# Optimization experiments

Hardware: AMD Instinct MI355X
Metric: run time of the kernel (lower is better)

The kernel has to match this reference:

```python
import jax, jax.numpy as jnp
import numpy as np

N_NODES = 100000
N_EDGES = 1600000
IN_DIM, HID, N_CLS = 128, 256, 40


def setup_inputs() -> dict:
    key = jax.random.key(0)
    ks = jax.random.split(key, 8)
    x = jax.random.normal(ks[0], (N_NODES, IN_DIM), dtype=jnp.float32)
    edge_index = jax.random.randint(ks[1], (2, N_EDGES), 0, N_NODES, dtype=jnp.int64)
    def glorot(k, shape):
        scale = (6.0 / (shape[0] + shape[1])) ** 0.5
        return jax.random.uniform(k, shape, jnp.float32, -scale, scale)
    return {
        "x": x,
        "edge_index": edge_index,
        "W1": glorot(ks[2], (IN_DIM, HID)),
        "b1": jnp.zeros((HID,), jnp.float32),
        "W2": glorot(ks[3], (HID, HID)),
        "b2": jnp.zeros((HID,), jnp.float32),
        "W3": glorot(ks[4], (HID, N_CLS)),
        "b3": jnp.zeros((N_CLS,), jnp.float32),
    }


def _gcn_norm(edge_index, num_nodes):
    # Add self-loops, then symmetric normalization deg^-1/2 * deg^-1/2 (PyG GCNConv).
    loops = jnp.arange(num_nodes, dtype=edge_index.dtype)
    src = jnp.concatenate([edge_index[0], loops])
    dst = jnp.concatenate([edge_index[1], loops])
    deg = jax.ops.segment_sum(jnp.ones_like(dst, dtype=jnp.float32), dst,
                              num_segments=num_nodes)
    dinv = jnp.where(deg > 0, jax.lax.rsqrt(deg), 0.0)
    norm = dinv[src] * dinv[dst]  # [E + N]
    return src, dst, norm


def _gcn_conv(x, W, b, src, dst, norm, num_nodes):
    h = x @ W                       # [N, out] dense GEMM first (out <= in here is fine)
    msg = h[src] * norm[:, None]    # irregular gather, [E+N, out]
    out = jax.ops.segment_sum(msg, dst, num_segments=num_nodes)  # scatter-add
    return out + b


def reference(x, edge_index, W1, b1, W2, b2, W3, b3):
    n = x.shape[0]
    src, dst, norm = _gcn_norm(edge_index, n)
    h = jax.nn.relu(_gcn_conv(x, W1, b1, src, dst, norm, n))
    h = jax.nn.relu(_gcn_conv(h, W2, b2, src, dst, norm, n))
    h = _gcn_conv(h, W3, b3, src, dst, norm, n)
    return jax.nn.log_softmax(h, axis=1)
```

## Files before the change

kernel.cpp:

```cpp
#include <hip/hip_runtime.h>
#include <stdint.h>
#include <math.h>

#define N_NODES 100000
#define N_EDGES 1600000
#define IN_DIM 128
#define HID 256
#define N_CLS 40
#define NBKT 391
#define NPB 391

typedef __attribute__((ext_vector_type(8))) short short8;
typedef __attribute__((ext_vector_type(4))) float f32x4;

__device__ __forceinline__ unsigned short f2bf(float f) {
  unsigned b = __float_as_uint(f);
  b += 0x7fffu + ((b >> 16) & 1u);
  return (unsigned short)(b >> 16);
}
__device__ __forceinline__ float bflo(unsigned u) { return __uint_as_float(u << 16); }
__device__ __forceinline__ float bfhi(unsigned u) { return __uint_as_float(u & 0xffff0000u); }

__device__ __forceinline__ int load_idx(const void* eidx, int flag, size_t pos) {
  return flag ? (int)((const long long*)eidx)[pos] : ((const int*)eidx)[pos];
}

__global__ __launch_bounds__(512) void k_pre0(const unsigned int* __restrict__ ew,
                                              int* __restrict__ flag,
                                              int* __restrict__ hist) {
  int t = threadIdx.x;
  for (int k = t; k < NBKT; k += 512) hist[k] = 0;
  __shared__ unsigned int sh[512];
  unsigned int v = 0;
  for (int k = t; k < 4096; k += 512) v |= ew[2 * k + 1];
  sh[t] = v;
  __syncthreads();
  for (int s = 256; s > 0; s >>= 1) {
    if (t < s) sh[t] |= sh[t + s];
    __syncthreads();
  }
  if (t == 0) flag[0] = (sh[0] == 0u) ? 1 : 0;
}

__global__ __launch_bounds__(256) void k_hist(const void* __restrict__ eidx,
                                              const int* __restrict__ flagp,
                                              int* __restrict__ hist) {
  __shared__ int lh[NBKT];
  int t = threadIdx.x;
  for (int k = t; k < NBKT; k += 256) lh[k] = 0;
  __syncthreads();
  int flag = flagp[0];
  int base = blockIdx.x * 4096;
#pragma unroll
  for (int j = 0; j < 16; j++) {
    int e = base + j * 256 + t;
    if (e < N_EDGES) {
      int d = load_idx(eidx, flag, (size_t)N_EDGES + e);
      atomicAdd(&lh[d >> 8], 1);
    }
  }
  __syncthreads();
  for (int k = t; k < NBKT; k += 256) {
    int c = lh[k];
    if (c) atomicAdd(&hist[k], c);
  }
}

__global__ __launch_bounds__(512) void k_bscan(const int* __restrict__ hist,
                                               int* __restrict__ bucket_start,
                                               int* __restrict__ bucket_cursor) {
  __shared__ int sh[512];
  int t = threadIdx.x;
  int v = (t < NBKT) ? hist[t] : 0;
  sh[t] = v;
  __syncthreads();
  for (int off = 1; off < 512; off <<= 1) {
    int u = (t >= off) ? sh[t - off] : 0;
    __syncthreads();
    sh[t] += u;
    __syncthreads();
  }
  if (t < NBKT) {
    bucket_start[t + 1] = sh[t];
    bucket_cursor[t] = sh[t] - v;
  }
  if (t == 0) bucket_start[0] = 0;
}

__global__ __launch_bounds__(256) void k_part(const void* __restrict__ eidx,
                                              const int* __restrict__ flagp,
                                              int* __restrict__ bucket_cursor,
                                              uint2* __restrict__ bpairs) {
  __shared__ int lcur[NBKT];
  int t = threadIdx.x;
  for (int k = t; k < NBKT; k += 256) lcur[k] = 0;
  __syncthreads();
  int flag = flagp[0];
  int base = blockIdx.x * 4096;
#pragma unroll
  for (int j = 0; j < 16; j++) {
    int e = base + j * 256 + t;
    if (e < N_EDGES) {
      int d = load_idx(eidx, flag, (size_t)N_EDGES + e);
      atomicAdd(&lcur[d >> 8], 1);
    }
  }
  __syncthreads();
  for (int k = t; k < NBKT; k += 256) {
    int c = lcur[k];
    int g = c ? atomicAdd(&bucket_cursor[k], c) : 0;
    lcur[k] = g;
  }
  __syncthreads();
#pragma unroll
  for (int j = 0; j < 16; j++) {
    int e = base + j * 256 + t;
    if (e < N_EDGES) {
      int s = load_idx(eidx, flag, e);
      int d = load_idx(eidx, flag, (size_t)N_EDGES + e);
      int p = atomicAdd(&lcur[d >> 8], 1);
      bpairs[p] = make_uint2((unsigned)s, (unsigned)d);
    }
  }
}

__global__ __launch_bounds__(256) void k_bsort(const uint2* __restrict__ bpairs,
                                               const int* __restrict__ bucket_start,
                                               int* __restrict__ row_start,
                                               float* __restrict__ dinv,
                                               int* __restrict__ csr_src) {
  __shared__ int ldeg[256], lsum[256], lcur[256];
  int b = blockIdx.x, t = threadIdx.x;
  int d0 = b << 8;
  int nd = min(256, N_NODES - d0);
  int base = bucket_start[b];
  int n = bucket_start[b + 1] - base;
  ldeg[t] = 0;
  __syncthreads();
  for (int i = t; i < n; i += 256) {
    uint2 p = bpairs[base + i];
    atomicAdd(&ldeg[p.y - d0], 1);
  }
  __syncthreads();
  lsum[t] = ldeg[t];
  __syncthreads();
  for (int off = 1; off < 256; off <<= 1) {
    int v = (t >= off) ? lsum[t - off] : 0;
    __syncthreads();
    lsum[t] += v;
    __syncthreads();
  }
  int excl = lsum[t] - ldeg[t];
  if (t < nd) {
    row_start[d0 + t] = base + excl;
    dinv[d0 + t] = rsqrtf((float)(ldeg[t] + 1));
  }
  lcur[t] = base + excl;
  __syncthreads();
  for (int i = t; i < n; i += 256) {
    uint2 p = bpairs[base + i];
    int pos = atomicAdd(&lcur[p.y - d0], 1);
    csr_src[pos] = (int)p.x;
  }
  if (b == 0 && t == 0) row_start[N_NODES] = N_EDGES;
}

__global__ __launch_bounds__(256) void k_wprep(const float* __restrict__ W1,
                                               const float* __restrict__ W2,
                                               const float* __restrict__ W3,
                                               unsigned short* __restrict__ T1,
                                               unsigned short* __restrict__ T2,
                                               unsigned short* __restrict__ T3) {
  int idx = blockIdx.x * 256 + threadIdx.x;
  if (idx < 32768) {
    int n = idx >> 7, k = idx & 127;
    T1[idx] = f2bf(W1[(size_t)k * HID + n]);
  } else if (idx < 98304) {
    int j = idx - 32768;
    int n = j >> 8, k = j & 255;
    T2[j] = f2bf(W2[(size_t)k * HID + n]);
  } else if (idx < 131072) {
    int j = idx - 98304;
    int n = j >> 8, k = j & 255;
    T3[j] = f2bf((n < N_CLS) ? W3[(size_t)k * N_CLS + n] : 0.f);
  }
}

__global__ __launch_bounds__(256) void k_qx(const float* __restrict__ x,
                                            const float* __restrict__ dinv,
                                            unsigned short* __restrict__ xq,
                                            float* __restrict__ sw_x) {
  int node = (blockIdx.x << 2) + (threadIdx.x >> 6);
  int lane = threadIdx.x & 63;
  if (node >= N_NODES) return;
  float2 v = ((const float2*)x)[(size_t)node * 64 + lane];
  float m = fmaxf(fabsf(v.x), fabsf(v.y));
  for (int off = 32; off; off >>= 1) m = fmaxf(m, __shfl_down(m, off));
  m = __shfl(m, 0);
  float inv = (m > 0.f) ? 127.f / m : 0.f;
  int q0 = __float2int_rn(v.x * inv);
  int q1 = __float2int_rn(v.y * inv);
  xq[(size_t)node * 64 + lane] = (unsigned short)((q0 & 0xff) | ((q1 & 0xff) << 8));
  if (lane == 0) sw_x[node] = dinv[node] * ((m > 0.f) ? m / 127.f : 0.f);
}

__device__ __forceinline__ void up4a(unsigned v, float w,
                                     float& a0, float& a1, float& a2, float& a3) {
  float f0, f1, f2, f3;
  asm("v_cvt_f32_ubyte0 %0, %1" : "=v"(f0) : "v"(v));
  asm("v_cvt_f32_ubyte1 %0, %1" : "=v"(f1) : "v"(v));
  asm("v_cvt_f32_ubyte2 %0, %1" : "=v"(f2) : "v"(v));
  asm("v_cvt_f32_ubyte3 %0, %1" : "=v"(f3) : "v"(v));
  a0 = fmaf(f0, w, a0);
  a1 = fmaf(f1, w, a1);
  a2 = fmaf(f2, w, a2);
  a3 = fmaf(f3, w, a3);
}

__global__ __launch_bounds__(256, 8) void k_agg256i(const unsigned* __restrict__ tbl,
                                                    uint2* __restrict__ out,
                                                    const float* __restrict__ dinv,
                                                    const float* __restrict__ swp,
                                                    const int* __restrict__ row_start,
                                                    const int* __restrict__ csr_src) {
  int node = (blockIdx.x << 2) + (threadIdx.x >> 6);
  int lane = threadIdx.x & 63;
  if (node >= N_NODES) return;
  node = __builtin_amdgcn_readfirstlane(node);
  const char* tb = (const char*)tbl;
  const char* sb = (const char*)swp;
  int l4 = lane << 2;
  int h4 = (lane >= 32) ? 4 : 0;
  float d = dinv[node];
  float ws = *(const float*)(sb + ((size_t)(unsigned)node << 3) + h4);
  unsigned v0 = *(const unsigned*)(tb + ((size_t)(unsigned)node << 8) + l4);
  float a0 = 0.f, a1 = 0.f, a2 = 0.f, a3 = 0.f;

  int e0 = __builtin_amdgcn_readfirstlane(row_start[node]);
  int e1 = __builtin_amdgcn_readfirstlane(row_start[node + 1]);
  const int* ep = csr_src + e0;
  int n = e1 - e0;

  int idx[8];
  if (n > 0) {
#pragma unroll
    for (int j = 0; j < 8; j++) idx[j] = __builtin_amdgcn_readfirstlane(ep[min(j, n - 1)]);
  }
  up4a(v0, ws, a0, a1, a2, a3);

  int k = 0;
  for (; k + 8 <= n; k += 8) {
    int cur[8];
#pragma unroll
    for (int j = 0; j < 8; j++) cur[j] = idx[j];
    if (k + 8 < n) {
#pragma unroll
      for (int j = 0; j < 8; j++)
        idx[j] = __builtin_amdgcn_readfirstlane(ep[min(k + 8 + j, n - 1)]);
    }
    unsigned r[8];
    float w[8];
#pragma unroll
    for (int j = 0; j < 8; j++)
      r[j] = *(const unsigned*)(tb + ((size_t)(unsigned)cur[j] << 8) + l4);
#pragma unroll
    for (int j = 0; j < 8; j++)
      w[j] = *(const float*)(sb + ((size_t)(unsigned)cur[j] << 3) + h4);
#pragma unroll
    for (int j = 0; j < 8; j++) up4a(r[j], w[j], a0, a1, a2, a3);
  }
  if (k < n) {
    unsigned r[8];
    float w[8];
#pragma unroll
    for (int j = 0; j < 8; j++)
      r[j] = *(const unsigned*)(tb + ((size_t)(unsigned)idx[j] << 8) + l4);
#pragma unroll
    for (int j = 0; j < 8; j++) {
      float wv = *(const float*)(sb + ((size_t)(unsigned)idx[j] << 3) + h4);
      w[j] = (k + j < n) ? wv : 0.f;
    }
#pragma unroll
    for (int j = 0; j < 8; j++) up4a(r[j], w[j], a0, a1, a2, a3);
  }

  a0 *= d; a1 *= d; a2 *= d; a3 *= d;
  uint2 o;
  o.x = f2bf(a0) | ((unsigned)f2bf(a1) << 16);
  o.y = f2bf(a2) | ((unsigned)f2bf(a3) << 16);
  out[(size_t)node * 64 + lane] = o;
}

__global__ __launch_bounds__(256, 8) void k_agg128i(const unsigned short* __restrict__ tbl,
                                                    unsigned* __restrict__ out,
                                                    const float* __restrict__ dinv,
                                                    const float* __restrict__ sw,
                                                    const int* __restrict__ row_start,
                                                    const int* __restrict__ csr_src) {
  int node = (blockIdx.x << 2) + (threadIdx.x >> 6);
  int lane = threadIdx.x & 63;
  if (node >= N_NODES) return;
  node = __builtin_amdgcn_readfirstlane(node);
  const char* tb = (const char*)tbl;
  int l2 = lane << 1;
  float d = dinv[node];
  float ws = sw[node];
  unsigned short v0 = *(const unsigned short*)(tb + ((size_t)(unsigned)node << 7) + l2);

  int e0 = __builtin_amdgcn_readfirstlane(row_start[node]);
  int e1 = __builtin_amdgcn_readfirstlane(row_start[node + 1]);
  const int* ep = csr_src + e0;
  int n = e1 - e0;

  int idx[8];
  if (n > 0) {
#pragma unroll
    for (int j = 0; j < 8; j++) idx[j] = __builtin_amdgcn_readfirstlane(ep[min(j, n - 1)]);
  }
  float a0 = (float)(signed char)(v0 & 0xff) * ws;
  float a1 = (float)(signed char)(v0 >> 8) * ws;

  int k = 0;
  for (; k + 8 <= n; k += 8) {
    int cur[8];
#pragma unroll
    for (int j = 0; j < 8; j++) cur[j] = idx[j];
    if (k + 8 < n) {
#pragma unroll
      for (int j = 0; j < 8; j++)
        idx[j] = __builtin_amdgcn_readfirstlane(ep[min(k + 8 + j, n - 1)]);
    }
    unsigned short r[8];
    float w[8];
#pragma unroll
    for (int j = 0; j < 8; j++)
      r[j] = *(const unsigned short*)(tb + ((size_t)(unsigned)cur[j] << 7) + l2);
#pragma unroll
    for (int j = 0; j < 8; j++) w[j] = sw[cur[j]];
#pragma unroll
    for (int j = 0; j < 8; j++) {
      a0 = fmaf((float)(signed char)(r[j] & 0xff), w[j], a0);
      a1 = fmaf((float)(signed char)(r[j] >> 8), w[j], a1);
    }
  }
  if (k < n) {
    unsigned short r[8];
    float w[8];
#pragma unroll
    for (int j = 0; j < 8; j++)
      r[j] = *(const unsigned short*)(tb + ((size_t)(unsigned)idx[j] << 7) + l2);
#pragma unroll
    for (int j = 0; j < 8; j++) {
      float wv = sw[idx[j]];
      w[j] = (k + j < n) ? wv : 0.f;
    }
#pragma unroll
    for (int j = 0; j < 8; j++) {
      a0 = fmaf((float)(signed char)(r[j] & 0xff), w[j], a0);
      a1 = fmaf((float)(signed char)(r[j] >> 8), w[j], a1);
    }
  }

  a0 *= d; a1 *= d;
  out[(size_t)node * 64 + lane] = f2bf(a0) | ((unsigned)f2bf(a1) << 16);
}

__global__ __launch_bounds__(256) void k_gemm_bres(const unsigned short* __restrict__ A,
                                                   int lda,
                                                   const unsigned short* __restrict__ B,
                                                   const float* __restrict__ bias,
                                                   unsigned short* __restrict__ C, int ldc,
                                                   int M, int relu) {
  __shared__ alignas(16) char smem[65536];
  int tid = threadIdx.x;
  int lane = tid & 63, wv = tid >> 6;
  int quad = lane >> 4, li = lane & 15;
  int row0 = blockIdx.x * 128, col0 = blockIdx.y * 128;

  int ar0 = min(row0 + wv * 32 + li, M - 1);
  int ar1 = min(row0 + wv * 32 + 16 + li, M - 1);
  const short8* pA0 = (const short8*)(A + (size_t)ar0 * lda + quad * 8);
  const short8* pA1 = (const short8*)(A + (size_t)ar1 * lda + quad * 8);
  short8 a0 = pA0[0];
  short8 a1 = pA1[0];

  {
    const char* src = (const char*)(B + (size_t)col0 * 256);
#pragma unroll
    for (int it = 0; it < 16; it++) {
      int i = tid + it * 256;
      int r = i >> 5, c = i & 31;
      *(short8*)(smem + (((r << 9) + (c << 4)) ^ ((r & 7) << 4))) =
          *(const short8*)(src + ((size_t)r << 9) + (c << 4));
    }
  }
  __syncthreads();

  f32x4 acc[2][8];
#pragma unroll
  for (int i = 0; i < 2; i++)
#pragma unroll
    for (int j = 0; j < 8; j++) acc[i][j] = 0.f;

#pragma unroll
  for (int kc = 0; kc < 8; kc++) {
    short8 b[8];
#pragma unroll
    for (int ni = 0; ni < 8; ni++) {
      int brow = ni * 16 + li;
      b[ni] = *(const short8*)(smem +
          (((brow << 9) + (kc << 6) + (quad << 4)) ^ ((brow & 7) << 4)));
    }
    short8 ca0 = a0, ca1 = a1;
    if (kc < 7) {
      a0 = pA0[(kc + 1) * 4];
      a1 = pA1[(kc + 1) * 4];
    }
#pragma unroll
    for (int ni = 0; ni < 8; ni++) {
      acc[0][ni] = __builtin_amdgcn_mfma_f32_16x16x32_bf16(ca0, b[ni], acc[0][ni], 0, 0, 0);
      acc[1][ni] = __builtin_amdgcn_mfma_f32_16x16x32_bf16(ca1, b[ni], acc[1][ni], 0, 0, 0);
    }
  }

  __syncthreads();
  unsigned short (*Ct)[136] = (unsigned short (*)[136])smem;
#pragma unroll
  for (int mi = 0; mi < 2; mi++)
#pragma unroll
    for (int ni = 0; ni < 8; ni++) {
      int c = ni * 16 + li;
      float bz = bias ? bias[col0 + c] : 0.f;
#pragma unroll
      for (int r = 0; r < 4; r++) {
        int row = wv * 32 + mi * 16 + quad * 4 + r;
        float o = acc[mi][ni][r] + bz;
        if (relu) o = fmaxf(o, 0.f);
        Ct[row][c] = f2bf(o);
      }
    }
  __syncthreads();
  int vc8 = (ldc - col0 >= 128) ? 16 : 8;
  int total = 128 * vc8;
  for (int i = tid; i < total; i += 256) {
    int row = (vc8 == 16) ? (i >> 4) : (i >> 3);
    int ch = i & (vc8 - 1);
    int gr = row0 + row;
    if (gr < M)
      *(uint4*)(C + (size_t)gr * ldc + col0 + ch * 8) = *(const uint4*)&Ct[row][ch * 8];
  }
}

__global__ __launch_bounds__(256) void k_gemm_q(const unsigned short* __restrict__ A,
                                                int lda,
                                                const unsigned short* __restrict__ B,
                                                const float* __restrict__ bias,
                                                const float* __restrict__ dinv,
                                                unsigned* __restrict__ hq,
                                                float* __restrict__ sw_h,
                                                int M) {
  __shared__ alignas(16) char smem[32768];
  int tid = threadIdx.x;
  int lane = tid & 63, wv = tid >> 6;
  int quad = lane >> 4, li = lane & 15;
  int row0 = blockIdx.x * 128, col0 = blockIdx.y * 128;
  int half = blockIdx.y;

  int ar0 = min(row0 + wv * 32 + li, M - 1);
  int ar1 = min(row0 + wv * 32 + 16 + li, M - 1);
  const short8* pA0 = (const short8*)(A + (size_t)ar0 * lda + quad * 8);
  const short8* pA1 = (const short8*)(A + (size_t)ar1 * lda + quad * 8);
  short8 a0 = pA0[0];
  short8 a1 = pA1[0];

  {
    const char* src = (const char*)(B + (size_t)col0 * 128);
#pragma unroll
    for (int it = 0; it < 8; it++) {
      int i = tid + it * 256;
      int r = i >> 4, c = i & 15;
      *(short8*)(smem + (((r << 8) + (c << 4)) ^ ((r & 7) << 4))) =
          *(const short8*)(src + ((size_t)r << 8) + (c << 4));
    }
  }
  __syncthreads();

  f32x4 acc[2][8];
#pragma unroll
  for (int i = 0; i < 2; i++)
#pragma unroll
    for (int j = 0; j < 8; j++) acc[i][j] = 0.f;

#pragma unroll
  for (int kc = 0; kc < 4; kc++) {
    short8 b[8];
#pragma unroll
    for (int ni = 0; ni < 8; ni++) {
      int brow = ni * 16 + li;
      b[ni] = *(const short8*)(smem +
          (((brow << 8) + (kc << 6) + (quad << 4)) ^ ((brow & 7) << 4)));
    }
    short8 ca0 = a0, ca1 = a1;
    if (kc < 3) {
      a0 = pA0[(kc + 1) * 4];
      a1 = pA1[(kc + 1) * 4];
    }
#pragma unroll
    for (int ni = 0; ni < 8; ni++) {
      acc[0][ni] = __builtin_amdgcn_mfma_f32_16x16x32_bf16(ca0, b[ni], acc[0][ni], 0, 0, 0);
      acc[1][ni] = __builtin_amdgcn_mfma_f32_16x16x32_bf16(ca1, b[ni], acc[1][ni], 0, 0, 0);
    }
  }

#pragma unroll
  for (int ni = 0; ni < 8; ni++) {
    float bz = bias[col0 + ni * 16 + li];
#pragma unroll
    for (int mi = 0; mi < 2; mi++)
#pragma unroll
      for (int r = 0; r < 4; r++)
        acc[mi][ni][r] = fmaxf(acc[mi][ni][r] + bz, 0.f);
  }
  float m2[2][4];
#pragma unroll
  for (int mi = 0; mi < 2; mi++)
#pragma unroll
    for (int r = 0; r < 4; r++) {
      float m = acc[mi][0][r];
#pragma unroll
      for (int ni = 1; ni < 8; ni++) m = fmaxf(m, acc[mi][ni][r]);
      m2[mi][r] = m;
    }
#pragma unroll
  for (int st = 1; st < 16; st <<= 1)
#pragma unroll
    for (int mi = 0; mi < 2; mi++)
#pragma unroll
      for (int r = 0; r < 4; r++)
        m2[mi][r] = fmaxf(m2[mi][r], __shfl_xor(m2[mi][r], st));
  float rs[2][4];
#pragma unroll
  for (int mi = 0; mi < 2; mi++)
#pragma unroll
    for (int r = 0; r < 4; r++)
      rs[mi][r] = (m2[mi][r] > 0.f) ? 255.f / m2[mi][r] : 0.f;
  if (li == 0) {
#pragma unroll
    for (int mi = 0; mi < 2; mi++)
#pragma unroll
      for (int r = 0; r < 4; r++) {
        int grow = row0 + wv * 32 + mi * 16 + quad * 4 + r;
        if (grow < M)
          sw_h[(size_t)grow * 2 + half] =
              dinv[grow] * ((m2[mi][r] > 0.f) ? m2[mi][r] / 255.f : 0.f);
      }
  }
  __syncthreads();
  unsigned char (*qtile)[128] = (unsigned char (*)[128])smem;
#pragma unroll
  for (int mi = 0; mi < 2; mi++)
#pragma unroll
    for (int ni = 0; ni < 8; ni++) {
      int c = ni * 16 + li;
#pragma unroll
      for (int r = 0; r < 4; r++) {
        int row = wv * 32 + mi * 16 + quad * 4 + r;
        qtile[row][c] = (unsigned char)__float2uint_rn(acc[mi][ni][r] * rs[mi][r]);
      }
    }
  __syncthreads();
  const uint4* qt = (const uint4*)smem;
#pragma unroll
  for (int k = 0; k < 4; k++) {
    int idx = tid + k * 256;
    int row = idx >> 3, p = idx & 7;
    int grow = row0 + row;
    if (grow < M)
      *(uint4*)(hq + (size_t)grow * 64 + half * 32 + p * 4) = qt[idx];
  }
}

__global__ __launch_bounds__(256) void k_agg40_lsm(const unsigned* __restrict__ in,
                                                   float* __restrict__ out,
                                                   const float* __restrict__ dinv,
                                                   const int* __restrict__ row_start,
                                                   const int* __restrict__ csr_src,
                                                   const float* __restrict__ bias) {
  int node = (blockIdx.x << 2) + (threadIdx.x >> 6);
  int lane = threadIdx.x & 63;
  if (node >= N_NODES) return;
  int g = (lane >= 40) ? 2 : (lane >= 20 ? 1 : 0);
  int c = lane - g * 20;
  bool act3 = lane < 60;
  const unsigned* base = in + c;
  float d = dinv[node];
  float ws = (g == 0 && act3) ? d : 0.f;
  unsigned u0 = base[(size_t)node * 32];
  float a0 = bflo(u0) * ws, a1 = bfhi(u0) * ws;
  int e1 = row_start[node + 1];
  int eb = row_start[node];
  for (; eb + 12 <= e1; eb += 12) {
    int ea = eb + g, eb2 = eb + 3 + g, ec = eb + 6 + g, ed = eb + 9 + g;
    int ia = csr_src[ea], ib = csr_src[eb2], ic = csr_src[ec], id = csr_src[ed];
    float wa = act3 ? dinv[ia] : 0.f;
    float wb = act3 ? dinv[ib] : 0.f;
    float wc = act3 ? dinv[ic] : 0.f;
    float wd = act3 ? dinv[id] : 0.f;
    unsigned ra = base[(size_t)ia * 32];
    unsigned rb = base[(size_t)ib * 32];
    unsigned rc = base[(size_t)ic * 32];
    unsigned rd = base[(size_t)id * 32];
    a0 = fmaf(bflo(ra), wa, a0); a1 = fmaf(bfhi(ra), wa, a1);
    a0 = fmaf(bflo(rb), wb, a0); a1 = fmaf(bfhi(rb), wb, a1);
    a0 = fmaf(bflo(rc), wc, a0); a1 = fmaf(bfhi(rc), wc, a1);
    a0 = fmaf(bflo(rd), wd, a0); a1 = fmaf(bfhi(rd), wd, a1);
  }
  for (; eb < e1; eb += 3) {
    int ea = eb + g;
    bool v = act3 && (ea < e1);
    int ia = v ? csr_src[ea] : 0;
    float wa = v ? dinv[ia] : 0.f;
    unsigned ra = base[(size_t)ia * 32];
    a0 = fmaf(bflo(ra), wa, a0); a1 = fmaf(bfhi(ra), wa, a1);
  }
  a0 += __shfl(a0, c + 20) + __shfl(a0, c + 40);
  a1 += __shfl(a1, c + 20) + __shfl(a1, c + 40);
  bool act = lane < 20;
  float v0 = act ? a0 * d + bias[2 * lane] : -INFINITY;
  float v1 = act ? a1 * d + bias[2 * lane + 1] : -INFINITY;
  float m = fmaxf(v0, v1);
  for (int off = 32; off; off >>= 1) m = fmaxf(m, __shfl_down(m, off));
  m = __shfl(m, 0);
  float s = act ? expf(v0 - m) + expf(v1 - m) : 0.f;
  for (int off = 32; off; off >>= 1) s += __shfl_down(s, off);
  s = __shfl(s, 0);
  float lse = m + logf(s);
  if (act) {
    out[(size_t)node * N_CLS + 2 * lane] = v0 - lse;
    out[(size_t)node * N_CLS + 2 * lane + 1] = v1 - lse;
  }
}

extern "C" void kernel_launch(void* const* d_in, const int* in_sizes, int n_in,
                              void* d_out, int out_size, void* d_ws, size_t ws_size,
                              hipStream_t stream) {
  const float* x  = (const float*)d_in[0];
  const void*  ei = d_in[1];
  const float* W1 = (const float*)d_in[2];
  const float* b1 = (const float*)d_in[3];
  const float* W2 = (const float*)d_in[4];
  const float* b2 = (const float*)d_in[5];
  const float* W3 = (const float*)d_in[6];
  const float* b3 = (const float*)d_in[7];
  float* out = (float*)d_out;

  char* w = (char*)d_ws;
  auto alloc = [&](size_t bytes) {
    char* p = w;
    w += (bytes + 255) & ~(size_t)255;
    return p;
  };
  int*   flag          = (int*)alloc(64);
  int*   hist          = (int*)alloc((size_t)NBKT * 4);
  int*   bucket_start  = (int*)alloc((size_t)(NBKT + 1) * 4);
  int*   bucket_cursor = (int*)alloc((size_t)NBKT * 4);
  uint2* bpairs        = (uint2*)alloc((size_t)N_EDGES * 8);
  int*   csr_src       = (int*)alloc((size_t)N_EDGES * 4);
  int*   row_start     = (int*)alloc(((size_t)N_NODES + 1) * 4);
  float* dinv          = (float*)alloc((size_t)N_NODES * 4);
  float* sw_x          = (float*)alloc((size_t)N_NODES * 4);
  float* sw_h          = (float*)alloc((size_t)N_NODES * 2 * 4);
  unsigned short* Wt1  = (unsigned short*)alloc((size_t)HID * IN_DIM * 2);
  unsigned short* Wt2  = (unsigned short*)alloc((size_t)HID * HID * 2);
  unsigned short* Wt3  = (unsigned short*)alloc((size_t)128 * HID * 2);
  unsigned short* xq   = (unsigned short*)alloc((size_t)N_NODES * 64 * 2);
  unsigned*       hq   = (unsigned*)alloc((size_t)N_NODES * 64 * 4);
  char* R0 = alloc((size_t)N_NODES * HID * 2);
  char* R1 = alloc((size_t)N_NODES * HID * 2);

  unsigned*       aggX  = (unsigned*)R0;
  uint2*          aggH1 = (uint2*)R0;
  unsigned short* h2    = (unsigned short*)R1;
  unsigned short* C3    = (unsigned short*)R0;

  const int nb_w1 = (N_NODES + 3) / 4;
  const int gm    = (N_NODES + 127) / 128;

  k_pre0<<<1, 512, 0, stream>>>((const unsigned int*)ei, flag, hist);
  k_hist<<<NPB, 256, 0, stream>>>(ei, flag, hist);
  k_bscan<<<1, 512, 0, stream>>>(hist, bucket_start, bucket_cursor);
  k_part<<<NPB, 256, 0, stream>>>(ei, flag, bucket_cursor, bpairs);
  k_bsort<<<NBKT, 256, 0, stream>>>(bpairs, bucket_start, row_start, dinv, csr_src);

  k_wprep<<<512, 256, 0, stream>>>(W1, W2, W3, Wt1, Wt2, Wt3);
  k_qx<<<nb_w1, 256, 0, stream>>>(x, dinv, xq, sw_x);

  k_agg128i<<<nb_w1, 256, 0, stream>>>(xq, aggX, dinv, sw_x, row_start, csr_src);
  k_gemm_q<<<dim3(gm, 2), 256, 0, stream>>>((const unsigned short*)aggX, IN_DIM, Wt1, b1,
                                            dinv, hq, sw_h, N_NODES);
  k_agg256i<<<nb_w1, 256, 0, stream>>>(hq, aggH1, dinv, sw_h, row_start, csr_src);
  k_gemm_bres<<<dim3(gm, 2), 256, 0, stream>>>((const unsigned short*)aggH1, HID, Wt2, b2,
                                               h2, HID, N_NODES, 1);
  k_gemm_bres<<<dim3(gm, 1), 256, 0, stream>>>(h2, HID, Wt3, nullptr,
                                               C3, 64, N_NODES, 0);
  k_agg40_lsm<<<nb_w1, 256, 0, stream>>>((const unsigned*)C3, out, dinv, row_start,
                                         csr_src, b3);
}
```

Before: 483.5 us.

## Process two nodes per wavefront in int8 aggregation kernels for more memory parallelism

Each wavefront in the 128- and 256-wide quantized gather-aggregation kernels now handles two consecutive nodes. Their neighbor loops are interleaved so 16 independent row gathers are in flight per iteration instead of 8. Remainder loops and tails handle the case where the two nodes have unequal degree, and the grid is halved to match. The aim is more memory-level parallelism for the latency-bound gathers, at the cost of extra registers (which may lower occupancy) and more code paths for imbalanced degrees.

```diff
diff --git a/kernel.cpp b/kernel.cpp
--- a/kernel.cpp
+++ b/kernel.cpp
@@ -223,72 +223,159 @@
                                                     const float* __restrict__ swp,
                                                     const int* __restrict__ row_start,
                                                     const int* __restrict__ csr_src) {
-  int node = (blockIdx.x << 2) + (threadIdx.x >> 6);
   int lane = threadIdx.x & 63;
-  if (node >= N_NODES) return;
-  node = __builtin_amdgcn_readfirstlane(node);
+  int n0 = (blockIdx.x << 3) + ((threadIdx.x >> 6) << 1);
+  if (n0 >= N_NODES) return;
+  int nodeA = __builtin_amdgcn_readfirstlane(n0);
+  int nodeB = nodeA + 1;
+  bool hasB = (nodeB < N_NODES);
   const char* tb = (const char*)tbl;
   const char* sb = (const char*)swp;
   int l4 = lane << 2;
   int h4 = (lane >= 32) ? 4 : 0;
-  float d = dinv[node];
-  float ws = *(const float*)(sb + ((size_t)(unsigned)node << 3) + h4);
-  unsigned v0 = *(const unsigned*)(tb + ((size_t)(unsigned)node << 8) + l4);
-  float a0 = 0.f, a1 = 0.f, a2 = 0.f, a3 = 0.f;
-
-  int e0 = __builtin_amdgcn_readfirstlane(row_start[node]);
-  int e1 = __builtin_amdgcn_readfirstlane(row_start[node + 1]);
-  const int* ep = csr_src + e0;
-  int n = e1 - e0;
-
-  int idx[8];
-  if (n > 0) {
-#pragma unroll
-    for (int j = 0; j < 8; j++) idx[j] = __builtin_amdgcn_readfirstlane(ep[min(j, n - 1)]);
-  }
-  up4a(v0, ws, a0, a1, a2, a3);
-
-  int k = 0;
-  for (; k + 8 <= n; k += 8) {
-    int cur[8];
-#pragma unroll
-    for (int j = 0; j < 8; j++) cur[j] = idx[j];
-    if (k + 8 < n) {
+
+  float dA = dinv[nodeA];
+  float wsA = *(const float*)(sb + ((size_t)(unsigned)nodeA << 3) + h4);
+  unsigned v0A = *(const unsigned*)(tb + ((size_t)(unsigned)nodeA << 8) + l4);
+  float dB = 0.f, wsB = 0.f;
+  unsigned v0B = 0;
+  if (hasB) {
+    dB = dinv[nodeB];
+    wsB = *(const float*)(sb + ((size_t)(unsigned)nodeB << 3) + h4);
+    v0B = *(const unsigned*)(tb + ((size_t)(unsigned)nodeB << 8) + l4);
+  }
+
+  int eA0 = __builtin_amdgcn_readfirstlane(row_start[nodeA]);
+  int eM  = __builtin_amdgcn_readfirstlane(row_start[nodeA + 1]);
+  int eB1 = hasB ? __builtin_amdgcn_readfirstlane(row_start[nodeB + 1]) : eM;
+  const int* epA = csr_src + eA0;
+  const int* epB = csr_src + eM;
+  int na = eM - eA0;
+  int nb = eB1 - eM;
+
+  float aA0 = 0.f, aA1 = 0.f, aA2 = 0.f, aA3 = 0.f;
+  float aB0 = 0.f, aB1 = 0.f, aB2 = 0.f, aB3 = 0.f;
+
+  int idxA[8], idxB[8];
+  if (na > 0) {
+#pragma unroll
+    for (int j = 0; j < 8; j++) idxA[j] = __builtin_amdgcn_readfirstlane(epA[min(j, na - 1)]);
+  }
+  if (nb > 0) {
+#pragma unroll
+    for (int j = 0; j < 8; j++) idxB[j] = __builtin_amdgcn_readfirstlane(epB[min(j, nb - 1)]);
+  }
+  up4a(v0A, wsA, aA0, aA1, aA2, aA3);
+  up4a(v0B, wsB, aB0, aB1, aB2, aB3);
+
+  int kA = 0, kB = 0;
+  while (kA + 8 <= na && kB + 8 <= nb) {
+    unsigned rA[8], rB[8];
+    float wA[8], wB[8];
+#pragma unroll
+    for (int j = 0; j < 8; j++)
+      rA[j] = *(const unsigned*)(tb + ((size_t)(unsigned)idxA[j] << 8) + l4);
+#pragma unroll
+    for (int j = 0; j < 8; j++)
+      rB[j] = *(const unsigned*)(tb + ((size_t)(unsigned)idxB[j] << 8) + l4);
+#pragma unroll
+    for (int j = 0; j < 8; j++)
+      wA[j] = *(const float*)(sb + ((size_t)(unsigned)idxA[j] << 3) + h4);
+#pragma unroll
+    for (int j = 0; j < 8; j++)
+      wB[j] = *(const float*)(sb + ((size_t)(unsigned)idxB[j] << 3) + h4);
+    if (kA + 8 < na) {
 #pragma unroll
       for (int j = 0; j < 8; j++)
-        idx[j] = __builtin_amdgcn_readfirstlane(ep[min(k + 8 + j, n - 1)]);
-    }
+        idxA[j] = __builtin_amdgcn_readfirstlane(epA[min(kA + 8 + j, na - 1)]);
+    }
+    if (kB + 8 < nb) {
+#pragma unroll
+      for (int j = 0; j < 8; j++)
+        idxB[j] = __builtin_amdgcn_readfirstlane(epB[min(kB + 8 + j, nb - 1)]);
+    }
+#pragma unroll
+    for (int j = 0; j < 8; j++) up4a(rA[j], wA[j], aA0, aA1, aA2, aA3);
+#pragma unroll
+    for (int j = 0; j < 8; j++) up4a(rB[j], wB[j], aB0, aB1, aB2, aB3);
+    kA += 8;
+    kB += 8;
+  }
+  for (; kA + 8 <= na; kA += 8) {
     unsigned r[8];
     float w[8];
 #pragma unroll
     for (int j = 0; j < 8; j++)
-      r[j] = *(const unsigned*)(tb + ((size_t)(unsigned)cur[j] << 8) + l4);
-#pragma unroll
-    for (int j = 0; j < 8; j++)
-      w[j] = *(const float*)(sb + ((size_t)(unsigned)cur[j] << 3) + h4);
-#pragma unroll
-    for (int j = 0; j < 8; j++) up4a(r[j], w[j], a0, a1, a2, a3);
-  }
-  if (k < n) {
+      r[j] = *(const unsigned*)(tb + ((size_t)(unsigned)idxA[j] << 8) + l4);
+#pragma unroll
+    for (int j = 0; j < 8; j++)
+      w[j] = *(const float*)(sb + ((size_t)(unsigned)idxA[j] << 3) + h4);
+    if (kA + 8 < na) {
+#pragma unroll
+      for (int j = 0; j < 8; j++)
+        idxA[j] = __builtin_amdgcn_readfirstlane(epA[min(kA + 8 + j, na - 1)]);
+    }
+#pragma unroll
+    for (int j = 0; j < 8; j++) up4a(r[j], w[j], aA0, aA1, aA2, aA3);
+  }
+  for (; kB + 8 <= nb; kB += 8) {
     unsigned r[8];
     float w[8];
 #pragma unroll
     for (int j = 0; j < 8; j++)
-      r[j] = *(const unsigned*)(tb + ((size_t)(unsigned)idx[j] << 8) + l4);
-#pragma unroll
-    for (int j = 0; j < 8; j++) {
-      float wv = *(const float*)(sb + ((size_t)(unsigned)idx[j] << 3) + h4);
-      w[j] = (k + j < n) ? wv : 0.f;
-    }
-#pragma unroll
-    for (int j = 0; j < 8; j++) up4a(r[j], w[j], a0, a1, a2, a3);
-  }
-
-  a0 *= d; a1 *= d; a2 *= d; a3 *= d;
-  uint2 o;
-  o.x = f2bf(a0) | ((unsigned)f2bf(a1) << 16);
-  o.y = f2bf(a2) | ((unsigned)f2bf(a3) << 16);
-  out[(size_t)node * 64 + lane] = o;
+      r[j] = *(const unsigned*)(tb + ((size_t)(unsigned)idxB[j] << 8) + l4);
+#pragma unroll
+    for (int j = 0; j < 8; j++)
+      w[j] = *(const float*)(sb + ((size_t)(unsigned)idxB[j] << 3) + h4);
+    if (kB + 8 < nb) {
+#pragma unroll
+      for (int j = 0; j < 8; j++)
+        idxB[j] = __builtin_amdgcn_readfirstlane(epB[min(kB + 8 + j, nb - 1)]);
+    }
+#pragma unroll
+    for (int j = 0; j < 8; j++) up4a(r[j], w[j], aB0, aB1, aB2, aB3);
+  }
+  if (kA < na) {
+    unsigned r[8];
+    float w[8];
+#pragma unroll
+    for (int j = 0; j < 8; j++)
+      r[j] = *(const unsigned*)(tb + ((size_t)(unsigned)idxA[j] << 8) + l4);
+#pragma unroll
+    for (int j = 0; j < 8; j++) {
+      float wv = *(const float*)(sb + ((size_t)(unsigned)idxA[j] << 3) + h4);
+      w[j] = (kA + j < na) ? wv : 0.f;
+    }
+#pragma unroll
+    for (int j = 0; j < 8; j++) up4a(r[j], w[j], aA0, aA1, aA2, aA3);
+  }
+  if (kB < nb) {
+    unsigned r[8];
+    float w[8];
+#pragma unroll
+    for (int j = 0; j < 8; j++)
+      r[j] = *(const unsigned*)(tb + ((size_t)(unsigned)idxB[j] << 8) + l4);
+#pragma unroll
+    for (int j = 0; j < 8; j++) {
+      float wv = *(const float*)(sb + ((size_t)(unsigned)idxB[j] << 3) + h4);
+      w[j] = (kB + j < nb) ? wv : 0.f;
+    }
+#pragma unroll
+    for (int j = 0; j < 8; j++) up4a(r[j], w[j], aB0, aB1, aB2, aB3);
+  }
+
+  aA0 *= dA; aA1 *= dA; aA2 *= dA; aA3 *= dA;
+  uint2 oA;
+  oA.x = f2bf(aA0) | ((unsigned)f2bf(aA1) << 16);
+  oA.y = f2bf(aA2) | ((unsigned)f2bf(aA3) << 16);
+  out[(size_t)nodeA * 64 + lane] = oA;
+  if (hasB) {
+    aB0 *= dB; aB1 *= dB; aB2 *= dB; aB3 *= dB;
+    uint2 oB;
+    oB.x = f2bf(aB0) | ((unsigned)f2bf(aB1) << 16);
+    oB.y = f2bf(aB2) | ((unsigned)f2bf(aB3) << 16);
+    out[(size_t)nodeB * 64 + lane] = oB;
+  }
 }
 
 __global__ __launch_bounds__(256, 8) void k_agg128i(const unsigned short* __restrict__ tbl,
@@ -297,72 +384,164 @@
                                                     const float* __restrict__ sw,
                                                     const int* __restrict__ row_start,
                                                     const int* __restrict__ csr_src) {
-  int node = (blockIdx.x << 2) + (threadIdx.x >> 6);
   int lane = threadIdx.x & 63;
-  if (node >= N_NODES) return;
-  node = __builtin_amdgcn_readfirstlane(node);
+  int n0 = (blockIdx.x << 3) + ((threadIdx.x >> 6) << 1);
+  if (n0 >= N_NODES) return;
+  int nodeA = __builtin_amdgcn_readfirstlane(n0);
+  int nodeB = nodeA + 1;
+  bool hasB = (nodeB < N_NODES);
   const char* tb = (const char*)tbl;
   int l2 = lane << 1;
-  float d = dinv[node];
-  float ws = sw[node];
-  unsigned short v0 = *(const unsigned short*)(tb + ((size_t)(unsigned)node << 7) + l2);
-
-  int e0 = __builtin_amdgcn_readfirstlane(row_start[node]);
-  int e1 = __builtin_amdgcn_readfirstlane(row_start[node + 1]);
-  const int* ep = csr_src + e0;
-  int n = e1 - e0;
-
-  int idx[8];
-  if (n > 0) {
-#pragma unroll
-    for (int j = 0; j < 8; j++) idx[j] = __builtin_amdgcn_readfirstlane(ep[min(j, n - 1)]);
-  }
-  float a0 = (float)(signed char)(v0 & 0xff) * ws;
-  float a1 = (float)(signed char)(v0 >> 8) * ws;
-
-  int k = 0;
-  for (; k + 8 <= n; k += 8) {
-    int cur[8];
-#pragma unroll
-    for (int j = 0; j < 8; j++) cur[j] = idx[j];
-    if (k + 8 < n) {
+
+  float dA = dinv[nodeA];
+  float wsA = sw[nodeA];
+  unsigned short v0A = *(const unsigned short*)(tb + ((size_t)(unsigned)nodeA << 7) + l2);
+  float dB = 0.f, wsB = 0.f;
+  unsigned short v0B = 0;
+  if (hasB) {
+    dB = dinv[nodeB];
+    wsB = sw[nodeB];
+    v0B = *(const unsigned short*)(tb + ((size_t)(unsigned)nodeB << 7) + l2);
+  }
+
+  int eA0 = __builtin_amdgcn_readfirstlane(row_start[nodeA]);
+  int eM  = __builtin_amdgcn_readfirstlane(row_start[nodeA + 1]);
+  int eB1 = hasB ? __builtin_amdgcn_readfirstlane(row_start[nodeB + 1]) : eM;
+  const int* epA = csr_src + eA0;
+  const int* epB = csr_src + eM;
+  int na = eM - eA0;
+  int nb = eB1 - eM;
+
+  int idxA[8], idxB[8];
+  if (na > 0) {
+#pragma unroll
+    for (int j = 0; j < 8; j++) idxA[j] = __builtin_amdgcn_readfirstlane(epA[min(j, na - 1)]);
+  }
+  if (nb > 0) {
+#pragma unroll
+    for (int j = 0; j < 8; j++) idxB[j] = __builtin_amdgcn_readfirstlane(epB[min(j, nb - 1)]);
+  }
+  float aA0 = (float)(signed char)(v0A & 0xff) * wsA;
+  float aA1 = (float)(signed char)(v0A >> 8) * wsA;
+  float aB0 = (float)(signed char)(v0B & 0xff) * wsB;
+  float aB1 = (float)(signed char)(v0B >> 8) * wsB;
+
+  int kA = 0, kB = 0;
+  while (kA + 8 <= na && kB + 8 <= nb) {
+    unsigned short rA[8], rB[8];
+    float wA[8], wB[8];
+#pragma unroll
+    for (int j = 0; j < 8; j++)
+      rA[j] = *(const unsigned short*)(tb + ((size_t)(unsigned)idxA[j] << 7) + l2);
+#pragma unroll
+    for (int j = 0; j < 8; j++)
+      rB[j] = *(const unsigned short*)(tb + ((size_t)(unsigned)idxB[j] << 7) + l2);
+#pragma unroll
+    for (int j = 0; j < 8; j++) wA[j] = sw[idxA[j]];
+#pragma unroll
+    for (int j = 0; j < 8; j++) wB[j] = sw[idxB[j]];
+    if (kA + 8 < na) {
 #pragma unroll
       for (int j = 0; j < 8; j++)
-        idx[j] = __builtin_amdgcn_readfirstlane(ep[min(k + 8 + j, n - 1)]);
-    }
+        idxA[j] = __builtin_amdgcn_readfirstlane(epA[min(kA + 8 + j, na - 1)]);
+    }
+    if (kB + 8 < nb) {
+#pragma unroll
+      for (int j = 0; j < 8; j++)
+        idxB[j] = __builtin_amdgcn_readfirstlane(epB[min(kB + 8 + j, nb - 1)]);
+    }
+#pragma unroll
+    for (int j = 0; j < 8; j++) {
+      aA0 = fmaf((float)(signed char)(rA[j] & 0xff), wA[j], aA0);
+      aA1 = fmaf((float)(signed char)(rA[j] >> 8), wA[j], aA1);
+    }
+#pragma unroll
+    for (int j = 0; j < 8; j++) {
+      aB0 = fmaf((float)(signed char)(rB[j] & 0xff), wB[j], aB0);
+      aB1 = fmaf((float)(signed char)(rB[j] >> 8), wB[j], aB1);
+    }
+    kA += 8;
+    kB += 8;
+  }
+  for (; kA + 8 <= na; kA += 8) {
     unsigned short r[8];
     float w[8];
 #pragma unroll
     for (int j = 0; j < 8; j++)
-      r[j] = *(const unsigned short*)(tb + ((size_t)(unsigned)cur[j] << 7) + l2);
-#pragma unroll
-    for (int j = 0; j < 8; j++) w[j] = sw[cur[j]];
-#pragma unroll
-    for (int j = 0; j < 8; j++) {
-      a0 = fmaf((float)(signed char)(r[j] & 0xff), w[j], a0);
-      a1 = fmaf((float)(signed char)(r[j] >> 8), w[j], a1);
-    }
-  }
-  if (k < n) {
+      r[j] = *(const unsigned short*)(tb + ((size_t)(unsigned)idxA[j] << 7) + l2);
+#pragma unroll
+    for (int j = 0; j < 8; j++) w[j] = sw[idxA[j]];
+    if (kA + 8 < na) {
+#pragma unroll
+      for (int j = 0; j < 8; j++)
+        idxA[j] = __builtin_amdgcn_readfirstlane(epA[min(kA + 8 + j, na - 1)]);
+    }
+#pragma unroll
+    for (int j = 0; j < 8; j++) {
+      aA0 = fmaf((float)(signed char)(r[j] & 0xff), w[j], aA0);
+      aA1 = fmaf((float)(signed char)(r[j] >> 8), w[j], aA1);
+    }
+  }
+  for (; kB + 8 <= nb; kB += 8) {
     unsigned short r[8];
     float w[8];
 #pragma unroll
     for (int j = 0; j < 8; j++)
-      r[j] = *(const unsigned short*)(tb + ((size_t)(unsigned)idx[j] << 7) + l2);
-#pragma unroll
-    for (int j = 0; j < 8; j++) {
-      float wv = sw[idx[j]];
-      w[j] = (k + j < n) ? wv : 0.f;
-    }
-#pragma unroll
-    for (int j = 0; j < 8; j++) {
-      a0 = fmaf((float)(signed char)(r[j] & 0xff), w[j], a0);
-      a1 = fmaf((float)(signed char)(r[j] >> 8), w[j], a1);
-    }
-  }
-
-  a0 *= d; a1 *= d;
-  out[(size_t)node * 64 + lane] = f2bf(a0) | ((unsigned)f2bf(a1) << 16);
+      r[j] = *(const unsigned short*)(tb + ((size_t)(unsigned)idxB[j] << 7) + l2);
+#pragma unroll
+    for (int j = 0; j < 8; j++) w[j] = sw[idxB[j]];
+    if (kB + 8 < nb) {
+#pragma unroll
+      for (int j = 0; j < 8; j++)
+        idxB[j] = __builtin_amdgcn_readfirstlane(epB[min(kB + 8 + j, nb - 1)]);
+    }
+#pragma unroll
+    for (int j = 0; j < 8; j++) {
+      aB0 = fmaf((float)(signed char)(r[j] & 0xff), w[j], aB0);
+      aB1 = fmaf((float)(signed char)(r[j] >> 8), w[j], aB1);
+    }
+  }
+  if (kA < na) {
+    unsigned short r[8];
+    float w[8];
+#pragma unroll
+    for (int j = 0; j < 8; j++)
+      r[j] = *(const unsigned short*)(tb + ((size_t)(unsigned)idxA[j] << 7) + l2);
+#pragma unroll
+    for (int j = 0; j < 8; j++) {
+      float wv = sw[idxA[j]];
+      w[j] = (kA + j < na) ? wv : 0.f;
+    }
+#pragma unroll
+    for (int j = 0; j < 8; j++) {
+      aA0 = fmaf((float)(signed char)(r[j] & 0xff), w[j], aA0);
+      aA1 = fmaf((float)(signed char)(r[j] >> 8), w[j], aA1);
+    }
+  }
+  if (kB < nb) {
+    unsigned short r[8];
+    float w[8];
+#pragma unroll
+    for (int j = 0; j < 8; j++)
+      r[j] = *(const unsigned short*)(tb + ((size_t)(unsigned)idxB[j] << 7) + l2);
+#pragma unroll
+    for (int j = 0; j < 8; j++) {
+      float wv = sw[idxB[j]];
+      w[j] = (kB + j < nb) ? wv : 0.f;
+    }
+#pragma unroll
+    for (int j = 0; j < 8; j++) {
+      aB0 = fmaf((float)(signed char)(r[j] & 0xff), w[j], aB0);
+      aB1 = fmaf((float)(signed char)(r[j] >> 8), w[j], aB1);
+    }
+  }
+
+  aA0 *= dA; aA1 *= dA;
+  out[(size_t)nodeA * 64 + lane] = f2bf(aA0) | ((unsigned)f2bf(aA1) << 16);
+  if (hasB) {
+    aB0 *= dB; aB1 *= dB;
+    out[(size_t)nodeB * 64 + lane] = f2bf(aB0) | ((unsigned)f2bf(aB1) << 16);
+  }
 }
 
 __global__ __launch_bounds__(256) void k_gemm_bres(const unsigned short* __restrict__ A,
@@ -684,6 +863,7 @@
   unsigned short* C3    = (unsigned short*)R0;
 
   const int nb_w1 = (N_NODES + 3) / 4;
+  const int nb_w2 = (N_NODES + 7) / 8;
   const int gm    = (N_NODES + 127) / 128;
 
   k_pre0<<<1, 512, 0, stream>>>((const unsigned int*)ei, flag, hist);
@@ -695,10 +875,10 @@
   k_wprep<<<512, 256, 0, stream>>>(W1, W2, W3, Wt1, Wt2, Wt3);
   k_qx<<<nb_w1, 256, 0, stream>>>(x, dinv, xq, sw_x);
 
-  k_agg128i<<<nb_w1, 256, 0, stream>>>(xq, aggX, dinv, sw_x, row_start, csr_src);
+  k_agg128i<<<nb_w2, 256, 0, stream>>>(xq, aggX, dinv, sw_x, row_start, csr_src);
   k_gemm_q<<<dim3(gm, 2), 256, 0, stream>>>((const unsigned short*)aggX, IN_DIM, Wt1, b1,
                                             dinv, hq, sw_h, N_NODES);
-  k_agg256i<<<nb_w1, 256, 0, stream>>>(hq, aggH1, dinv, sw_h, row_start, csr_src);
+  k_agg256i<<<nb_w2, 256, 0, stream>>>(hq, aggH1, dinv, sw_h, row_start, csr_src);
   k_gemm_bres<<<dim3(gm, 2), 256, 0, stream>>>((const unsigned short*)aggH1, HID, Wt2, b2,
                                                h2, HID, N_NODES, 1);
   k_gemm_bres<<<dim3(gm, 1), 256, 0, stream>>>(h2, HID, Wt3, nullptr,
```

New measurement: 480.3 us. Within noise of the previous version (-0.6%).
